# Kernel tuning notes

Hardware: AMD Instinct MI355X
Metric: run time of the kernel (lower is better)

The kernel has to match this reference:

```python
import jax, jax.numpy as jnp
import numpy as np

B, S, D, H = 2, 2048, 1024, 16
DH = D // H  # 64


def setup_inputs() -> dict:
    key = jax.random.key(0)
    ks = jax.random.split(key, 9)
    scale = 0.02
    x = jax.random.normal(ks[0], (B, S, D), dtype=jnp.float32)
    # per-head QKV weights stacked over heads: [H, D, DH]
    Wq = jax.random.normal(ks[1], (H, D, DH), dtype=jnp.float32) * scale
    Wk = jax.random.normal(ks[2], (H, D, DH), dtype=jnp.float32) * scale
    Wv = jax.random.normal(ks[3], (H, D, DH), dtype=jnp.float32) * scale
    bq = jax.random.normal(ks[4], (H, DH), dtype=jnp.float32) * scale
    bk = jax.random.normal(ks[5], (H, DH), dtype=jnp.float32) * scale
    bv = jax.random.normal(ks[6], (H, DH), dtype=jnp.float32) * scale
    Wo = jax.random.normal(ks[7], (D, D), dtype=jnp.float32) * scale
    bo = jax.random.normal(ks[8], (D,), dtype=jnp.float32) * scale
    return {"x": x, "Wq": Wq, "bq": bq, "Wk": Wk, "bk": bk, "Wv": Wv, "bv": bv, "Wo": Wo, "bo": bo}


def reference(x, Wq, bq, Wk, bk, Wv, bv, Wo, bo):
    # per-head projections: [B, H, S, DH]
    q = jnp.einsum('bsd,hde->bhse', x, Wq) + bq[None, :, None, :]
    k = jnp.einsum('bsd,hde->bhse', x, Wk) + bk[None, :, None, :]
    v = jnp.einsum('bsd,hde->bhse', x, Wv) + bv[None, :, None, :]
    scores = jnp.einsum('bhse,bhte->bhst', q, k) / jnp.sqrt(jnp.float32(DH))
    probs = jax.nn.softmax(scores, axis=-1)  # [B, H, S, S]
    ctx = jnp.einsum('bhst,bhte->bhse', probs, v)  # [B, H, S, DH]
    # concat heads: [B, S, H*DH]
    ctx = jnp.transpose(ctx, (0, 2, 1, 3)).reshape(x.shape[0], x.shape[1], H * DH)
    out = ctx @ Wo + bo  # output projection; dropout p=0 -> identity
    return out
```

## Files before the change

kernel.cpp:

```cpp
#include <hip/hip_runtime.h>

typedef __attribute__((ext_vector_type(8))) short short8;
typedef __attribute__((ext_vector_type(2))) float f32x2;
typedef __attribute__((ext_vector_type(4))) float f32x4;
typedef __attribute__((ext_vector_type(16))) float f32x16;
typedef __attribute__((ext_vector_type(4))) unsigned short us4;
typedef unsigned short ushort;

typedef __attribute__((address_space(3))) void lds_void;
typedef __attribute__((address_space(1))) void gbl_void;

__device__ __forceinline__ ushort f2bf(float f) {
  unsigned u = __float_as_uint(f);
  u += 0x7fff + ((u >> 16) & 1);
  return (ushort)(u >> 16);
}

__global__ void cvt_x_kernel(const float* __restrict__ x, ushort* __restrict__ xb) {
  int i = (blockIdx.x * 256 + threadIdx.x) * 8;
  float4 a = *(const float4*)(x + i);
  float4 b = *(const float4*)(x + i + 4);
  ushort o[8];
  o[0] = f2bf(a.x); o[1] = f2bf(a.y); o[2] = f2bf(a.z); o[3] = f2bf(a.w);
  o[4] = f2bf(b.x); o[5] = f2bf(b.y); o[6] = f2bf(b.z); o[7] = f2bf(b.w);
  *(short8*)(xb + i) = *(short8*)o;
}

__global__ void wprep_kernel(const float* __restrict__ Wq, const float* __restrict__ Wk,
                             const float* __restrict__ Wv, const float* __restrict__ Wo,
                             ushort* __restrict__ wqkv_t, ushort* __restrict__ wo_t) {
  __shared__ float T[64][65];
  const int k0 = blockIdx.x * 64;
  const int hy = blockIdx.y;
  const int m = blockIdx.z;
  const float* src = (m == 0) ? Wq : (m == 1) ? Wk : (m == 2) ? Wv : Wo;
#pragma unroll
  for (int it = 0; it < 16; ++it) {
    int idx = it * 256 + threadIdx.x;
    int kk = idx >> 6, e = idx & 63;
    float v = (m < 3) ? src[hy * 65536 + (k0 + kk) * 64 + e]
                      : src[(k0 + kk) * 1024 + hy * 64 + e];
    T[e][kk] = v;
  }
  __syncthreads();
  ushort* dst = (m < 3) ? (wqkv_t + (size_t)(m * 1024 + hy * 64) * 1024)
                        : (wo_t + (size_t)(hy * 64) * 1024);
#pragma unroll
  for (int it = 0; it < 2; ++it) {
    int c = it * 256 + threadIdx.x;
    int e = c >> 3, kc = (c & 7) * 8;
    ushort o[8];
#pragma unroll
    for (int j = 0; j < 8; ++j) o[j] = f2bf(T[e][kc + j]);
    *(short8*)&dst[(size_t)e * 1024 + k0 + kc] = *(short8*)o;
  }
}

__global__ __launch_bounds__(512, 2) void gemm_qkv256(
    const ushort* __restrict__ A, const ushort* __restrict__ Bt,
    const float* __restrict__ b0, const float* __restrict__ b1, const float* __restrict__ b2,
    ushort* __restrict__ qfp, ushort* __restrict__ kfp, ushort* __restrict__ vfp) {
  __shared__ ushort sm[3][2][256][32];
  const int tid = threadIdx.x;
  const int lane = tid & 63;
  const int wave = tid >> 6;
  const int l15 = lane & 15, l4 = lane >> 4;
  const int wwr = wave >> 2, wc = wave & 3;
  const int p0 = blockIdx.x;
  const int p = (p0 & 7) * 24 + (p0 >> 3);
  const int by = p & 15, bx = p >> 4;
  const int row0 = by * 256, col0 = bx * 256;

  const ushort* Ag = A + (size_t)row0 * 1024;
  const ushort* Bg = Bt + (size_t)col0 * 1024;
  char* smb = (char*)&sm[0][0][0][0];

  auto stage = [&](int buf, int kt, int c0) {
    const int c = c0 + tid;
    const int row = (c & 1023) >> 2;
    const int slot = c & 3;
    const int scol = (slot ^ ((row >> 1) & 3)) * 8;
    const ushort* src = ((c >> 10) ? Bg : Ag) + (size_t)row * 1024 + kt * 32 + scol;
    __builtin_amdgcn_global_load_lds((const gbl_void*)src,
        (lds_void*)(smb + buf * 32768 + (c0 + (tid & ~63)) * 16), 16, 0, 0);
  };
  auto rdA = [&](int buf, int mfg) {
    const int row = wwr * 128 + mfg * 16 + l15;
    return *(const short8*)(smb + buf * 32768 + row * 64 + ((l4 ^ ((row >> 1) & 3)) << 4));
  };
  auto rdB = [&](int buf, int nf) {
    const int row = wc * 64 + nf * 16 + l15;
    return *(const short8*)(smb + buf * 32768 + 16384 + row * 64 + ((l4 ^ ((row >> 1) & 3)) << 4));
  };

  f32x4 acc[8][4];
#pragma unroll
  for (int i = 0; i < 8; ++i)
#pragma unroll
    for (int j = 0; j < 4; ++j) acc[i][j] = (f32x4){0.f, 0.f, 0.f, 0.f};

  stage(0, 0, 0); stage(0, 0, 512); stage(0, 0, 1024); stage(0, 0, 1536);
  stage(1, 1, 0); stage(1, 1, 512); stage(1, 1, 1024); stage(1, 1, 1536);

  int buf = 0;
  for (int kt = 0; kt < 32; ++kt) {
    if (kt == 31) asm volatile("s_waitcnt vmcnt(0)" ::: "memory");
    else          asm volatile("s_waitcnt vmcnt(4)" ::: "memory");
    asm volatile("s_barrier" ::: "memory");
    const int kn = kt + 2;
    const int bn = (buf >= 1) ? buf - 1 : buf + 2;
    short8 bfr[4], af[4];
#pragma unroll
    for (int nf = 0; nf < 4; ++nf) bfr[nf] = rdB(buf, nf);
#pragma unroll
    for (int mf = 0; mf < 4; ++mf) af[mf] = rdA(buf, mf);
    if (kn < 32) { stage(bn, kn, 0); stage(bn, kn, 512); }
    __builtin_amdgcn_s_setprio(1);
#pragma unroll
    for (int mf = 0; mf < 4; ++mf)
#pragma unroll
      for (int nf = 0; nf < 4; ++nf)
        acc[mf][nf] = __builtin_amdgcn_mfma_f32_16x16x32_bf16(af[mf], bfr[nf], acc[mf][nf], 0, 0, 0);
    __builtin_amdgcn_s_setprio(0);
    asm volatile("s_barrier" ::: "memory");
#pragma unroll
    for (int mf = 0; mf < 4; ++mf) af[mf] = rdA(buf, 4 + mf);
    if (kn < 32) { stage(bn, kn, 1024); stage(bn, kn, 1536); }
    __builtin_amdgcn_s_setprio(1);
#pragma unroll
    for (int mf = 0; mf < 4; ++mf)
#pragma unroll
      for (int nf = 0; nf < 4; ++nf)
        acc[4 + mf][nf] = __builtin_amdgcn_mfma_f32_16x16x32_bf16(af[mf], bfr[nf], acc[4 + mf][nf], 0, 0, 0);
    __builtin_amdgcn_s_setprio(0);
    buf = (buf == 2) ? 0 : buf + 1;
  }

  const float QSCALE = 0.18033688f;
#pragma unroll
  for (int mfg = 0; mfg < 8; ++mfg) {
    const int row = row0 + wwr * 128 + mfg * 16 + l4 * 4;
    const int bb = row >> 11, s = row & 2047;
#pragma unroll
    for (int nf = 0; nf < 4; ++nf) {
      const int col = col0 + wc * 64 + nf * 16 + l15;
      if (col < 2048) {
        const int cf = col & 1023;
        const int h = cf >> 6, d = cf & 63;
        const int bh = bb * 16 + h;
        ushort* dst = (col < 1024) ? qfp : kfp;
        const float bias = ((col < 1024) ? b0 : b1)[cf];
        const float sc = (col < 1024) ? QSCALE : 1.0f;
        const size_t base =
            ((((size_t)bh * 64 + (s >> 5)) * 4 + (d >> 4)) * 64 + ((d >> 3) & 1) * 32 + (s & 31)) * 8 +
            (d & 7);
#pragma unroll
        for (int r = 0; r < 4; ++r) dst[base + r * 8] = f2bf((acc[mfg][nf][r] + bias) * sc);
      } else {
        const int ef = col - 2048;
        const int h = ef >> 6, e = ef & 63;
        const int bh = bb * 16 + h;
        const float bias = b2[ef];
        ushort o4[4];
#pragma unroll
        for (int r = 0; r < 4; ++r) o4[r] = f2bf(acc[mfg][nf][r] + bias);
        const size_t addr =
            ((((size_t)bh * 2 + (e >> 5)) * 128 + (s >> 4)) * 64 + ((s >> 3) & 1) * 32 + (e & 31)) * 8 +
            (s & 7);
        *(us4*)&vfp[addr] = *(us4*)o4;
      }
    }
  }
}

__global__ __launch_bounds__(256) void gemm_out_kernel(
    const ushort* __restrict__ A, const ushort* __restrict__ Bt,
    const float* __restrict__ b0, float* __restrict__ C) {
  __shared__ ushort sm[3][2][128][32];
  const int tid = threadIdx.x;
  const int lane = tid & 63;
  const int wave = tid >> 6;
  const int l15 = lane & 15, l4 = lane >> 4;
  const int wr = wave >> 1, wc = wave & 1;
  const int row0 = blockIdx.y * 128, col0 = blockIdx.x * 128;

  const ushort* Ag = A + (size_t)row0 * 1024;
  const ushort* Bg = Bt + (size_t)col0 * 1024;
  char* smb = (char*)&sm[0][0][0][0];

  auto stage = [&](int buf, int kt, int c0) {
    const int c = c0 + tid;
    const int row = (c & 511) >> 2;
    const int slot = c & 3;
    const int scol = (slot ^ ((row >> 1) & 3)) * 8;
    const ushort* src = ((c >> 9) ? Bg : Ag) + (size_t)row * 1024 + kt * 32 + scol;
    __builtin_amdgcn_global_load_lds((const gbl_void*)src,
        (lds_void*)(smb + buf * 16384 + (c0 + (tid & ~63)) * 16), 16, 0, 0);
  };
  auto rdA = [&](int buf, int mf) {
    const int row = wr * 64 + mf * 16 + l15;
    return *(const short8*)(smb + buf * 16384 + row * 64 + ((l4 ^ ((row >> 1) & 3)) << 4));
  };
  auto rdB = [&](int buf, int nf) {
    const int row = wc * 64 + nf * 16 + l15;
    return *(const short8*)(smb + buf * 16384 + 8192 + row * 64 + ((l4 ^ ((row >> 1) & 3)) << 4));
  };

  f32x4 acc[4][4];
#pragma unroll
  for (int i = 0; i < 4; ++i)
#pragma unroll
    for (int j = 0; j < 4; ++j) acc[i][j] = (f32x4){0.f, 0.f, 0.f, 0.f};

  stage(0, 0, 0); stage(0, 0, 256); stage(0, 0, 512); stage(0, 0, 768);
  stage(1, 1, 0); stage(1, 1, 256); stage(1, 1, 512); stage(1, 1, 768);

  int buf = 0;
  for (int kt = 0; kt < 32; ++kt) {
    if (kt == 31) asm volatile("s_waitcnt vmcnt(0)" ::: "memory");
    else          asm volatile("s_waitcnt vmcnt(4)" ::: "memory");
    asm volatile("s_barrier" ::: "memory");
    const int kn = kt + 2;
    const int bn = (buf >= 1) ? buf - 1 : buf + 2;
    short8 af[4], bfr[4];
#pragma unroll
    for (int nf = 0; nf < 4; ++nf) bfr[nf] = rdB(buf, nf);
#pragma unroll
    for (int mf = 0; mf < 4; ++mf) af[mf] = rdA(buf, mf);
    if (kn < 32) { stage(bn, kn, 0); stage(bn, kn, 256); stage(bn, kn, 512); stage(bn, kn, 768); }
    __builtin_amdgcn_s_setprio(1);
#pragma unroll
    for (int mf = 0; mf < 4; ++mf)
#pragma unroll
      for (int nf = 0; nf < 4; ++nf)
        acc[mf][nf] = __builtin_amdgcn_mfma_f32_16x16x32_bf16(af[mf], bfr[nf], acc[mf][nf], 0, 0, 0);
    __builtin_amdgcn_s_setprio(0);
    buf = (buf == 2) ? 0 : buf + 1;
  }

#pragma unroll
  for (int i = 0; i < 4; ++i) {
    const int row = row0 + wr * 64 + i * 16 + l4 * 4;
#pragma unroll
    for (int j = 0; j < 4; ++j) {
      const int col = col0 + wc * 64 + j * 16 + l15;
      const float bias = b0[col];
#pragma unroll
      for (int r = 0; r < 4; ++r)
        C[(size_t)(row + r) * 1024 + col] = acc[i][j][r] + bias;
    }
  }
}

__global__ __launch_bounds__(512, 2) void attn_kernel(const ushort* __restrict__ qf,
                                                      const ushort* __restrict__ kf,
                                                      const ushort* __restrict__ vf,
                                                      ushort* __restrict__ ctx) {
  __shared__ ushort sm[2][2][8192];
  const int tid = threadIdx.x;
  const int lane = tid & 63, wave = tid >> 6;
  const int grp = wave >> 2, gw = wave & 3;
  const int gtid = tid & 255;
  const int l31 = lane & 31, hi = lane >> 5;
  const int p0 = blockIdx.x;
  const int idx = p0 >> 3;
  const int bh = (p0 & 7) * 4 + (idx >> 4);
  const int q0 = ((idx & 15) * 4 + gw) * 32;
  const int b = bh >> 4, h = bh & 15;

  const size_t bhbase = (size_t)bh * 131072;
  const ushort* qfb = qf + bhbase + (size_t)(q0 >> 5) * 2048 + (size_t)lane * 8;
  char* gsm = (char*)&sm[grp][0][0];
  char* dbase = gsm + (gtid & ~63) * 16;

  short8 qb[4];
#pragma unroll
  for (int kk = 0; kk < 4; ++kk)
    qb[kk] = *(const short8*)(qfb + kk * 512);

  const int tbase = grp * 1024;
  const ushort* kp = kf + bhbase + (size_t)(tbase >> 5) * 2048 + gtid * 8;
  const ushort* vp = vf + bhbase + (size_t)(tbase >> 4) * 512 + gtid * 8;

  auto stage2 = [&](int buf, const ushort* kpp, const ushort* vpp) {
    char* d = dbase + buf * 16384;
    __builtin_amdgcn_global_load_lds((const gbl_void*)kpp, (lds_void*)(d), 16, 0, 0);
    __builtin_amdgcn_global_load_lds((const gbl_void*)(kpp + 2048), (lds_void*)(d + 4096), 16, 0, 0);
    __builtin_amdgcn_global_load_lds((const gbl_void*)(vpp), (lds_void*)(d + 8192), 16, 0, 0);
    __builtin_amdgcn_global_load_lds((const gbl_void*)(vpp + 65536), (lds_void*)(d + 12288), 16, 0, 0);
  };

  f32x16 cacc[2];
#pragma unroll
  for (int me = 0; me < 2; ++me)
#pragma unroll
    for (int r = 0; r < 16; ++r) cacc[me][r] = 0.f;
  f32x16 fz;
#pragma unroll
  for (int r = 0; r < 16; ++r) fz[r] = 0.f;
  f32x2 l2a = {0.f, 0.f}, l2b = {0.f, 0.f}, l2c = {0.f, 0.f}, l2d = {0.f, 0.f};

  stage2(0, kp, vp);
  for (int it = 0; it < 16; ++it) {
    asm volatile("s_waitcnt vmcnt(0)" ::: "memory");
    asm volatile("s_barrier" ::: "memory");
    if (it < 15) stage2((it + 1) & 1, kp + 4096, vp + 2048);
    kp += 4096; vp += 2048;

    const char* kb = gsm + (it & 1) * 16384;
    const char* vb = kb + 8192;

    short8 ka[2][4];
#pragma unroll
    for (int me = 0; me < 2; ++me)
#pragma unroll
      for (int kk = 0; kk < 4; ++kk)
        ka[me][kk] = *(const short8*)(kb + me * 4096 + kk * 1024 + lane * 16);

    f32x16 sacc[2];
    __builtin_amdgcn_s_setprio(1);
#pragma unroll
    for (int me = 0; me < 2; ++me) {
      sacc[me] = __builtin_amdgcn_mfma_f32_32x32x16_bf16(ka[me][0], qb[0], fz, 0, 0, 0);
#pragma unroll
      for (int kk = 1; kk < 4; ++kk)
        sacc[me] = __builtin_amdgcn_mfma_f32_32x32x16_bf16(ka[me][kk], qb[kk], sacc[me], 0, 0, 0);
    }
    __builtin_amdgcn_s_setprio(0);

    unsigned w[2][8];
#pragma unroll
    for (int me = 0; me < 2; ++me) {
      f32x2 pq[8];
#pragma unroll
      for (int j = 0; j < 8; ++j) {
        pq[j][0] = __builtin_amdgcn_exp2f(sacc[me][2 * j]);
        pq[j][1] = __builtin_amdgcn_exp2f(sacc[me][2 * j + 1]);
      }
      asm("v_pk_add_f32 %0, %1, %2" : "=v"(l2a) : "v"(pq[0]), "v"(l2a));
      asm("v_pk_add_f32 %0, %1, %2" : "=v"(l2b) : "v"(pq[1]), "v"(l2b));
      asm("v_pk_add_f32 %0, %1, %2" : "=v"(l2c) : "v"(pq[2]), "v"(l2c));
      asm("v_pk_add_f32 %0, %1, %2" : "=v"(l2d) : "v"(pq[3]), "v"(l2d));
      asm("v_pk_add_f32 %0, %1, %2" : "=v"(l2a) : "v"(pq[4]), "v"(l2a));
      asm("v_pk_add_f32 %0, %1, %2" : "=v"(l2b) : "v"(pq[5]), "v"(l2b));
      asm("v_pk_add_f32 %0, %1, %2" : "=v"(l2c) : "v"(pq[6]), "v"(l2c));
      asm("v_pk_add_f32 %0, %1, %2" : "=v"(l2d) : "v"(pq[7]), "v"(l2d));
#pragma unroll
      for (int j = 0; j < 8; ++j)
        asm("v_cvt_pk_bf16_f32 %0, %1, %2" : "=v"(w[me][j]) : "v"(pq[j][0]), "v"(pq[j][1]));
    }

    unsigned pb[4][4];
#pragma unroll
    for (int me = 0; me < 2; ++me)
#pragma unroll
      for (int c = 0; c < 2; ++c) {
        unsigned a0 = w[me][4 * c + 0], a1 = w[me][4 * c + 1];
        unsigned b0r = w[me][4 * c + 2], b1r = w[me][4 * c + 3];
        asm("v_permlane32_swap_b32 %0, %1" : "+v"(a0), "+v"(b0r));
        asm("v_permlane32_swap_b32 %0, %1" : "+v"(a1), "+v"(b1r));
        const int kk = me * 2 + c;
        pb[kk][0] = a0; pb[kk][1] = a1; pb[kk][2] = b0r; pb[kk][3] = b1r;
      }

    short8 va[2][4];
#pragma unroll
    for (int mev = 0; mev < 2; ++mev)
#pragma unroll
      for (int kk = 0; kk < 4; ++kk)
        va[mev][kk] = *(const short8*)(vb + mev * 4096 + kk * 1024 + lane * 16);

    __builtin_amdgcn_s_setprio(1);
#pragma unroll
    for (int mev = 0; mev < 2; ++mev)
#pragma unroll
      for (int kk = 0; kk < 4; ++kk)
        cacc[mev] = __builtin_amdgcn_mfma_f32_32x32x16_bf16(va[mev][kk], *(const short8*)&pb[kk][0],
                                                            cacc[mev], 0, 0, 0);
    __builtin_amdgcn_s_setprio(0);
  }

  float l_run = (l2a[0] + l2a[1]) + (l2b[0] + l2b[1]) + (l2c[0] + l2c[1]) + (l2d[0] + l2d[1]);
  l_run += __shfl_xor(l_run, 32);
  __syncthreads();
  float* mb = (float*)&sm[0][0][0];
  if (grp == 1) {
#pragma unroll
    for (int mev = 0; mev < 2; ++mev)
#pragma unroll
      for (int r = 0; r < 16; ++r)
        mb[(mev * 16 + r) * 256 + gw * 64 + lane] = cacc[mev][r];
    mb[8192 + gw * 64 + lane] = l_run;
  }
  __syncthreads();
  if (grp == 0) {
    const float l1 = mb[8192 + gw * 64 + lane];
    const float inv = 1.f / (l_run + l1);
    const int q = q0 + l31;
#pragma unroll
    for (int mev = 0; mev < 2; ++mev)
#pragma unroll
      for (int g = 0; g < 4; ++g) {
        ushort o4[4];
#pragma unroll
        for (int rr = 0; rr < 4; ++rr) {
          const int r = g * 4 + rr;
          const float v = (cacc[mev][r] + mb[(mev * 16 + r) * 256 + gw * 64 + lane]) * inv;
          o4[rr] = f2bf(v);
        }
        const int e0 = mev * 32 + 8 * g + 4 * hi;
        *(us4*)&ctx[(size_t)(b * 2048 + q) * 1024 + h * 64 + e0] = *(us4*)o4;
      }
  }
}

extern "C" void kernel_launch(void* const* d_in, const int* in_sizes, int n_in,
                              void* d_out, int out_size, void* d_ws, size_t ws_size,
                              hipStream_t stream) {
  const float* x = (const float*)d_in[0];
  const float* Wq = (const float*)d_in[1];
  const float* bq = (const float*)d_in[2];
  const float* Wk = (const float*)d_in[3];
  const float* bk = (const float*)d_in[4];
  const float* Wv = (const float*)d_in[5];
  const float* bv = (const float*)d_in[6];
  const float* Wo = (const float*)d_in[7];
  const float* bo = (const float*)d_in[8];
  float* out = (float*)d_out;

  char* ws = (char*)d_ws;
  ushort* xb = (ushort*)ws;
  ushort* ctx = xb;
  ushort* wqkv_t = (ushort*)(ws + 8u * 1024 * 1024);
  ushort* wo_t = (ushort*)(ws + 14u * 1024 * 1024);
  ushort* qf = (ushort*)(ws + 16u * 1024 * 1024);
  ushort* kf = (ushort*)(ws + 24u * 1024 * 1024);
  ushort* vf = (ushort*)(ws + 32u * 1024 * 1024);

  cvt_x_kernel<<<dim3(2048), dim3(256), 0, stream>>>(x, xb);
  wprep_kernel<<<dim3(16, 16, 4), dim3(256), 0, stream>>>(Wq, Wk, Wv, Wo, wqkv_t, wo_t);
  gemm_qkv256<<<dim3(192), dim3(512), 0, stream>>>(xb, wqkv_t, bq, bk, bv, qf, kf, vf);
  attn_kernel<<<dim3(512), dim3(512), 0, stream>>>(qf, kf, vf, ctx);
  gemm_out_kernel<<<dim3(8, 32), dim3(256), 0, stream>>>(ctx, wo_t, bo, out);
}
```

Before: 111.9 us.

## Load V fragments directly from global and merge prep kernels

The attention kernel stops staging V tiles through LDS with global_load_lds and instead loads V MFMA operands straight from global memory into registers at the top of each iteration. This halves LDS use per block and may allow more occupancy. In exchange, global latency now sits directly on the loop's critical path. Separately, the x conversion and weight transpose kernels are fused into one launch to save a kernel launch.

```diff
diff --git a/kernel.cpp b/kernel.cpp
--- a/kernel.cpp
+++ b/kernel.cpp
@@ -16,23 +16,28 @@
   return (ushort)(u >> 16);
 }
 
-__global__ void cvt_x_kernel(const float* __restrict__ x, ushort* __restrict__ xb) {
-  int i = (blockIdx.x * 256 + threadIdx.x) * 8;
-  float4 a = *(const float4*)(x + i);
-  float4 b = *(const float4*)(x + i + 4);
-  ushort o[8];
-  o[0] = f2bf(a.x); o[1] = f2bf(a.y); o[2] = f2bf(a.z); o[3] = f2bf(a.w);
-  o[4] = f2bf(b.x); o[5] = f2bf(b.y); o[6] = f2bf(b.z); o[7] = f2bf(b.w);
-  *(short8*)(xb + i) = *(short8*)o;
-}
-
-__global__ void wprep_kernel(const float* __restrict__ Wq, const float* __restrict__ Wk,
-                             const float* __restrict__ Wv, const float* __restrict__ Wo,
-                             ushort* __restrict__ wqkv_t, ushort* __restrict__ wo_t) {
+__global__ void prep_kernel(const float* __restrict__ x, const float* __restrict__ Wq,
+                            const float* __restrict__ Wk, const float* __restrict__ Wv,
+                            const float* __restrict__ Wo, ushort* __restrict__ xb,
+                            ushort* __restrict__ wqkv_t, ushort* __restrict__ wo_t) {
+  const int m = blockIdx.z;
+  if (m == 4) {
+    const int tn = (blockIdx.y * 16 + blockIdx.x) * 256 + threadIdx.x;
+#pragma unroll
+    for (int r = 0; r < 8; ++r) {
+      const int i = (tn + r * 65536) * 8;
+      float4 a = *(const float4*)(x + i);
+      float4 bb = *(const float4*)(x + i + 4);
+      ushort o[8];
+      o[0] = f2bf(a.x); o[1] = f2bf(a.y); o[2] = f2bf(a.z); o[3] = f2bf(a.w);
+      o[4] = f2bf(bb.x); o[5] = f2bf(bb.y); o[6] = f2bf(bb.z); o[7] = f2bf(bb.w);
+      *(short8*)(xb + i) = *(short8*)o;
+    }
+    return;
+  }
   __shared__ float T[64][65];
   const int k0 = blockIdx.x * 64;
   const int hy = blockIdx.y;
-  const int m = blockIdx.z;
   const float* src = (m == 0) ? Wq : (m == 1) ? Wk : (m == 2) ? Wv : Wo;
 #pragma unroll
   for (int it = 0; it < 16; ++it) {
@@ -256,7 +261,8 @@
                                                       const ushort* __restrict__ kf,
                                                       const ushort* __restrict__ vf,
                                                       ushort* __restrict__ ctx) {
-  __shared__ ushort sm[2][2][8192];
+  __shared__ ushort smK[2][2][4096];
+  __shared__ float lbuf[256];
   const int tid = threadIdx.x;
   const int lane = tid & 63, wave = tid >> 6;
   const int grp = wave >> 2, gw = wave & 3;
@@ -270,8 +276,8 @@
 
   const size_t bhbase = (size_t)bh * 131072;
   const ushort* qfb = qf + bhbase + (size_t)(q0 >> 5) * 2048 + (size_t)lane * 8;
-  char* gsm = (char*)&sm[grp][0][0];
-  char* dbase = gsm + (gtid & ~63) * 16;
+  const ushort* vb0 = vf + bhbase + (size_t)lane * 8;
+  char* gsm = (char*)&smK[grp][0][0];
 
   short8 qb[4];
 #pragma unroll
@@ -280,14 +286,11 @@
 
   const int tbase = grp * 1024;
   const ushort* kp = kf + bhbase + (size_t)(tbase >> 5) * 2048 + gtid * 8;
-  const ushort* vp = vf + bhbase + (size_t)(tbase >> 4) * 512 + gtid * 8;
-
-  auto stage2 = [&](int buf, const ushort* kpp, const ushort* vpp) {
-    char* d = dbase + buf * 16384;
-    __builtin_amdgcn_global_load_lds((const gbl_void*)kpp, (lds_void*)(d), 16, 0, 0);
+
+  auto stageK = [&](int buf, const ushort* kpp) {
+    char* d = gsm + buf * 8192 + (gtid & ~63) * 16;
+    __builtin_amdgcn_global_load_lds((const gbl_void*)kpp, (lds_void*)d, 16, 0, 0);
     __builtin_amdgcn_global_load_lds((const gbl_void*)(kpp + 2048), (lds_void*)(d + 4096), 16, 0, 0);
-    __builtin_amdgcn_global_load_lds((const gbl_void*)(vpp), (lds_void*)(d + 8192), 16, 0, 0);
-    __builtin_amdgcn_global_load_lds((const gbl_void*)(vpp + 65536), (lds_void*)(d + 12288), 16, 0, 0);
   };
 
   f32x16 cacc[2];
@@ -300,16 +303,22 @@
   for (int r = 0; r < 16; ++r) fz[r] = 0.f;
   f32x2 l2a = {0.f, 0.f}, l2b = {0.f, 0.f}, l2c = {0.f, 0.f}, l2d = {0.f, 0.f};
 
-  stage2(0, kp, vp);
+  stageK(0, kp);
   for (int it = 0; it < 16; ++it) {
     asm volatile("s_waitcnt vmcnt(0)" ::: "memory");
     asm volatile("s_barrier" ::: "memory");
-    if (it < 15) stage2((it + 1) & 1, kp + 4096, vp + 2048);
-    kp += 4096; vp += 2048;
-
-    const char* kb = gsm + (it & 1) * 16384;
-    const char* vb = kb + 8192;
-
+    if (it < 15) stageK((it + 1) & 1, kp + 4096);
+    kp += 4096;
+
+    const int tv = (tbase + it * 64) >> 4;
+    short8 va[2][4];
+#pragma unroll
+    for (int mev = 0; mev < 2; ++mev)
+#pragma unroll
+      for (int kk = 0; kk < 4; ++kk)
+        va[mev][kk] = *(const short8*)(vb0 + (size_t)(mev * 128 + tv + kk) * 512);
+
+    const char* kb = gsm + (it & 1) * 8192;
     short8 ka[2][4];
 #pragma unroll
     for (int me = 0; me < 2; ++me)
@@ -363,13 +372,6 @@
         pb[kk][0] = a0; pb[kk][1] = a1; pb[kk][2] = b0r; pb[kk][3] = b1r;
       }
 
-    short8 va[2][4];
-#pragma unroll
-    for (int mev = 0; mev < 2; ++mev)
-#pragma unroll
-      for (int kk = 0; kk < 4; ++kk)
-        va[mev][kk] = *(const short8*)(vb + mev * 4096 + kk * 1024 + lane * 16);
-
     __builtin_amdgcn_s_setprio(1);
 #pragma unroll
     for (int mev = 0; mev < 2; ++mev)
@@ -383,18 +385,18 @@
   float l_run = (l2a[0] + l2a[1]) + (l2b[0] + l2b[1]) + (l2c[0] + l2c[1]) + (l2d[0] + l2d[1]);
   l_run += __shfl_xor(l_run, 32);
   __syncthreads();
-  float* mb = (float*)&sm[0][0][0];
+  float* mb = (float*)&smK[0][0][0];
   if (grp == 1) {
 #pragma unroll
     for (int mev = 0; mev < 2; ++mev)
 #pragma unroll
       for (int r = 0; r < 16; ++r)
         mb[(mev * 16 + r) * 256 + gw * 64 + lane] = cacc[mev][r];
-    mb[8192 + gw * 64 + lane] = l_run;
+    lbuf[gw * 64 + lane] = l_run;
   }
   __syncthreads();
   if (grp == 0) {
-    const float l1 = mb[8192 + gw * 64 + lane];
+    const float l1 = lbuf[gw * 64 + lane];
     const float inv = 1.f / (l_run + l1);
     const int q = q0 + l31;
 #pragma unroll
@@ -437,8 +439,7 @@
   ushort* kf = (ushort*)(ws + 24u * 1024 * 1024);
   ushort* vf = (ushort*)(ws + 32u * 1024 * 1024);
 
-  cvt_x_kernel<<<dim3(2048), dim3(256), 0, stream>>>(x, xb);
-  wprep_kernel<<<dim3(16, 16, 4), dim3(256), 0, stream>>>(Wq, Wk, Wv, Wo, wqkv_t, wo_t);
+  prep_kernel<<<dim3(16, 16, 5), dim3(256), 0, stream>>>(x, Wq, Wk, Wv, Wo, xb, wqkv_t, wo_t);
   gemm_qkv256<<<dim3(192), dim3(512), 0, stream>>>(xb, wqkv_t, bq, bk, bv, qf, kf, vf);
   attn_kernel<<<dim3(512), dim3(512), 0, stream>>>(qf, kf, vf, ctx);
   gemm_out_kernel<<<dim3(8, 32), dim3(256), 0, stream>>>(ctx, wo_t, bo, out);
```

Result: slower. 119.8 us (+7.0%).
